# Optimization experiments

Hardware: AMD Instinct MI355X
Metric: run time of the kernel (lower is better)

The kernel has to match this reference:

```python
import jax, jax.numpy as jnp
import numpy as np

N_NODES = 50000
N_EDGES = 800000
IN_DIM = 128
HEADS = 8
HEAD_DIM = 16


def setup_inputs() -> dict:
    key = jax.random.key(0)
    ks = jax.random.split(key, 9)
    s = 1.0 / np.sqrt(IN_DIM)
    return {
        "h": jax.random.normal(ks[0], (N_NODES, IN_DIM), dtype=jnp.float32),
        "src": jax.random.randint(ks[1], (N_EDGES,), 0, N_NODES, dtype=jnp.int32),
        "dst": jax.random.randint(ks[2], (N_EDGES,), 0, N_NODES, dtype=jnp.int32),
        "WQ": jax.random.normal(ks[3], (IN_DIM, HEADS * HEAD_DIM), dtype=jnp.float32) * s,
        "bQ": jnp.zeros((HEADS * HEAD_DIM,), dtype=jnp.float32),
        "WK": jax.random.normal(ks[4], (IN_DIM, HEADS * HEAD_DIM), dtype=jnp.float32) * s,
        "bK": jnp.zeros((HEADS * HEAD_DIM,), dtype=jnp.float32),
        "WV": jax.random.normal(ks[5], (IN_DIM, HEADS * HEAD_DIM), dtype=jnp.float32) * s,
        "bV": jnp.zeros((HEADS * HEAD_DIM,), dtype=jnp.float32),
    }


def reference(h, src, dst, WQ, bQ, WK, bK, WV, bV):
    N = h.shape[0]
    sqrt_d = jnp.float32(np.sqrt(HEAD_DIM))
    # node projections, viewed as [N, H, D]
    Q = (h @ WQ + bQ).reshape(N, HEADS, HEAD_DIM)
    K = (h @ WK + bK).reshape(N, HEADS, HEAD_DIM)
    V = (h @ WV + bV).reshape(N, HEADS, HEAD_DIM)
    # edge scores: (K_src . Q_dst) per head, scaled exp with clamp [-5, 5]
    score = jnp.sum(K[src] * Q[dst], axis=-1, keepdims=True)  # [E, H, 1]
    score = jnp.exp(jnp.clip(score / sqrt_d, -5.0, 5.0))
    # segment-softmax denominator z and weighted V sum wV, both scattered to dst
    z = jax.ops.segment_sum(score, dst, num_segments=N)            # [N, H, 1]
    wV = jax.ops.segment_sum(V[src] * score, dst, num_segments=N)  # [N, H, D]
    # possible_empty: divide only where z > 0 (wV is 0 there anyway)
    head_out = jnp.where(z > 0, wV / jnp.where(z > 0, z, 1.0), wV)
    return head_out
```

## Files before the change

kernel.cpp:

```cpp
#include <hip/hip_runtime.h>
#include <math.h>

#define DIM 128
#define N_HEADS 8
#define HD 16
#define CAP 64

typedef __attribute__((ext_vector_type(8))) short bf16x8;
typedef __attribute__((ext_vector_type(4))) float f32x4;

__device__ __forceinline__ unsigned bf16pack2(float a, float b) {
    unsigned ua = __builtin_bit_cast(unsigned, a);
    unsigned ub = __builtin_bit_cast(unsigned, b);
    ua = (ua + 0x7FFFu + ((ua >> 16) & 1u)) >> 16;
    ub = (ub + 0x7FFFu + ((ub >> 16) & 1u)) >> 16;
    return ua | (ub << 16);
}
__device__ __forceinline__ float bf16lo(unsigned p) {
    return __builtin_bit_cast(float, p << 16);
}
__device__ __forceinline__ float bf16hi(unsigned p) {
    return __builtin_bit_cast(float, p & 0xFFFF0000u);
}

__global__ __launch_bounds__(256)
void init_kernel(const float* __restrict__ WQ, const float* __restrict__ bQ,
                 const float* __restrict__ WK, const float* __restrict__ bK,
                 const float* __restrict__ WV, const float* __restrict__ bV,
                 unsigned short* __restrict__ WT, float* __restrict__ bias384,
                 int* __restrict__ cnt, int NB, int N)
{
    if ((int)blockIdx.x < NB) {
        int i = blockIdx.x * 256 + threadIdx.x;
        if (i < N) cnt[i] = 0;
    } else {
        int idx = ((int)blockIdx.x - NB) * 256 + threadIdx.x;
        int c = idx >> 7, k = idx & 127;
        const float* W; const float* b; int col = c & 127;
        if (c < 128)      { W = WQ; b = bQ; }
        else if (c < 256) { W = WK; b = bK; }
        else              { W = WV; b = bV; }
        float v = W[k * DIM + col];
        WT[(size_t)c * DIM + k] = (unsigned short)(bf16pack2(v, 0.0f) & 0xFFFFu);
        if (k == 0) bias384[c] = b[col];
    }
}

__global__ __launch_bounds__(256)
void append_qkv_kernel(const int* __restrict__ src, const int* __restrict__ dst,
                       int* __restrict__ cnt, unsigned short* __restrict__ srcsF,
                       int E, int EB,
                       const float* __restrict__ h,
                       const unsigned short* __restrict__ WT,
                       const float* __restrict__ bias384,
                       unsigned* __restrict__ Qd, unsigned* __restrict__ KVd,
                       int N)
{
    __shared__ unsigned short hs[64 * 136];

    if ((int)blockIdx.x < EB) {
        int t = (blockIdx.x * 256 + threadIdx.x) * 4;
        if (t + 3 < E) {
            int4 d4 = *(const int4*)(dst + t);
            int4 s4 = *(const int4*)(src + t);
            int sl0 = atomicAdd(&cnt[d4.x], 1);
            int sl1 = atomicAdd(&cnt[d4.y], 1);
            int sl2 = atomicAdd(&cnt[d4.z], 1);
            int sl3 = atomicAdd(&cnt[d4.w], 1);
            if (sl0 < CAP) srcsF[(size_t)d4.x * CAP + sl0] = (unsigned short)s4.x;
            if (sl1 < CAP) srcsF[(size_t)d4.y * CAP + sl1] = (unsigned short)s4.y;
            if (sl2 < CAP) srcsF[(size_t)d4.z * CAP + sl2] = (unsigned short)s4.z;
            if (sl3 < CAP) srcsF[(size_t)d4.w * CAP + sl3] = (unsigned short)s4.w;
        } else {
            for (int e = t; e < E; ++e) {
                int d    = dst[e];
                int slot = atomicAdd(&cnt[d], 1);
                if (slot < CAP) srcsF[(size_t)d * CAP + slot] = (unsigned short)src[e];
            }
        }
        return;
    }

    const int tid = threadIdx.x;
    const int n0  = ((int)blockIdx.x - EB) * 64;

    #pragma unroll
    for (int i = 0; i < 4; ++i) {
        int lin  = i * 256 + tid;
        int node = lin >> 4;
        int k0   = (lin & 15) * 8;
        int gn   = n0 + node;
        float4 a0, a1;
        if (gn < N) {
            a0 = *(const float4*)(h + (size_t)gn * DIM + k0);
            a1 = *(const float4*)(h + (size_t)gn * DIM + k0 + 4);
        } else {
            a0 = make_float4(0.f, 0.f, 0.f, 0.f);
            a1 = a0;
        }
        uint4 p = make_uint4(bf16pack2(a0.x, a0.y), bf16pack2(a0.z, a0.w),
                             bf16pack2(a1.x, a1.y), bf16pack2(a1.z, a1.w));
        *(uint4*)(hs + node * 136 + k0) = p;
    }
    __syncthreads();

    const int wave   = tid >> 6;
    const int l      = tid & 63;
    const int lane16 = l & 15;
    const int quad   = l >> 4;
    const int wc0    = wave * 96;

    f32x4 acc[6][4];
    #pragma unroll
    for (int ct = 0; ct < 6; ++ct) {
        float4 bv = *(const float4*)(bias384 + wc0 + ct * 16 + quad * 4);
        #pragma unroll
        for (int rt = 0; rt < 4; ++rt)
            acc[ct][rt] = (f32x4){bv.x, bv.y, bv.z, bv.w};
    }

    #pragma unroll
    for (int ks = 0; ks < 4; ++ks) {
        bf16x8 a[6], b[4];
        #pragma unroll
        for (int ct = 0; ct < 6; ++ct)
            a[ct] = *(const bf16x8*)(WT + (size_t)(wc0 + ct * 16 + lane16) * DIM
                                         + ks * 32 + quad * 8);
        #pragma unroll
        for (int rt = 0; rt < 4; ++rt)
            b[rt] = *(const bf16x8*)(hs + (rt * 16 + lane16) * 136 + ks * 32 + quad * 8);
        #pragma unroll
        for (int ct = 0; ct < 6; ++ct)
            #pragma unroll
            for (int rt = 0; rt < 4; ++rt)
                acc[ct][rt] = __builtin_amdgcn_mfma_f32_16x16x32_bf16(
                    a[ct], b[rt], acc[ct][rt], 0, 0, 0);
    }

    #pragma unroll
    for (int ct = 0; ct < 6; ++ct) {
        const int col = wc0 + ct * 16 + quad * 4;
        #pragma unroll
        for (int rt = 0; rt < 4; ++rt) {
            int gn = n0 + rt * 16 + lane16;
            if (gn >= N) continue;
            f32x4 v = acc[ct][rt];
            uint2 pr = make_uint2(bf16pack2(v[0], v[1]), bf16pack2(v[2], v[3]));
            if (col < 128) {
                *(uint2*)(Qd + (size_t)gn * 64 + (col >> 1)) = pr;
            } else if (col < 256) {
                int c = col - 128;
                *(uint2*)(KVd + (size_t)gn * 128 + ((c >> 3) * 8) + ((c & 4) >> 1)) = pr;
            } else {
                int c = col - 256;
                *(uint2*)(KVd + (size_t)gn * 128 + ((c >> 3) * 8) + 4 + ((c & 4) >> 1)) = pr;
            }
        }
    }
}

__device__ __forceinline__ void issue_chunk(
    const unsigned* __restrict__ KVd, int bkt, int degc, int eg, int slot, int c,
    uint4 (&K)[4], uint4 (&V)[4])
{
    #pragma unroll
    for (int j = 0; j < 4; ++j) {
        int ee = eg + j * 4 + slot;
        int s  = __shfl(bkt, ee);
        s      = (ee < degc) ? s : 0;
        const uint4* p = (const uint4*)(KVd + (size_t)s * 128 + c * 8);
        K[j] = p[0];
        V[j] = p[1];
    }
}

__device__ __forceinline__ void compute_chunk(
    const uint4 (&K)[4], const uint4 (&V)[4], int eg, int degc, int slot,
    float q0, float q1, float q2, float q3,
    float q4, float q5, float q6, float q7,
    float acc[8], float& zs)
{
    float d[4];
    #pragma unroll
    for (int j = 0; j < 4; ++j)
        d[j] = bf16lo(K[j].x) * q0 + bf16hi(K[j].x) * q1
             + bf16lo(K[j].y) * q2 + bf16hi(K[j].y) * q3
             + bf16lo(K[j].z) * q4 + bf16hi(K[j].z) * q5
             + bf16lo(K[j].w) * q6 + bf16hi(K[j].w) * q7;
    #pragma unroll
    for (int j = 0; j < 4; ++j) d[j] += __shfl_xor(d[j], 1);

    #pragma unroll
    for (int j = 0; j < 4; ++j) {
        float pc = fminf(fmaxf(d[j] * 0.25f, -5.0f), 5.0f);
        float w  = ((eg + j * 4 + slot) < degc) ? __expf(pc) : 0.0f;
        zs += w;
        acc[0] += w * bf16lo(V[j].x); acc[1] += w * bf16hi(V[j].x);
        acc[2] += w * bf16lo(V[j].y); acc[3] += w * bf16hi(V[j].y);
        acc[4] += w * bf16lo(V[j].z); acc[5] += w * bf16hi(V[j].z);
        acc[6] += w * bf16lo(V[j].w); acc[7] += w * bf16hi(V[j].w);
    }
}

__global__ __launch_bounds__(256, 4)
void aggregate_kernel(const int* __restrict__ cnt,
                      const unsigned short* __restrict__ srcsF,
                      const unsigned* __restrict__ Qd,
                      const unsigned* __restrict__ KVd,
                      float* __restrict__ out, int N)
{
    const int l      = threadIdx.x & 63;
    const int slot   = l >> 4;
    const int c      = l & 15;
    const int stride = gridDim.x * 4;

    int node = blockIdx.x * 4 + (threadIdx.x >> 6);
    if (node >= N) return;

    int   deg = cnt[node];
    uint4 qd  = *(const uint4*)(Qd + (size_t)node * 64 + c * 4);
    int   bkt = srcsF[(size_t)node * CAP + l];

    uint4 K0[4], V0[4];
    issue_chunk(KVd, bkt, deg > CAP ? CAP : deg, 0, slot, c, K0, V0);

    for (;;) {
        const int  nn      = node + stride;
        const bool hasNext = nn < N;

        int ndeg = 0; uint4 nqd = make_uint4(0u, 0u, 0u, 0u); int nbkt = 0;
        if (hasNext) {
            ndeg = cnt[nn];
            nqd  = *(const uint4*)(Qd + (size_t)nn * 64 + c * 4);
            nbkt = srcsF[(size_t)nn * CAP + l];
        }

        const int degc = deg > CAP ? CAP : deg;

        uint4 K1[4], V1[4];
        const bool has1 = degc > 16;
        if (has1) issue_chunk(KVd, bkt, degc, 16, slot, c, K1, V1);

        const float q0 = bf16lo(qd.x), q1 = bf16hi(qd.x);
        const float q2 = bf16lo(qd.y), q3 = bf16hi(qd.y);
        const float q4 = bf16lo(qd.z), q5 = bf16hi(qd.z);
        const float q6 = bf16lo(qd.w), q7 = bf16hi(qd.w);

        float acc[8] = {0.f, 0.f, 0.f, 0.f, 0.f, 0.f, 0.f, 0.f};
        float zs = 0.f;

        compute_chunk(K0, V0, 0, degc, slot, q0, q1, q2, q3, q4, q5, q6, q7, acc, zs);
        if (has1)
            compute_chunk(K1, V1, 16, degc, slot, q0, q1, q2, q3, q4, q5, q6, q7, acc, zs);
        if (degc > 32) {
            issue_chunk(KVd, bkt, degc, 32, slot, c, K1, V1);
            compute_chunk(K1, V1, 32, degc, slot, q0, q1, q2, q3, q4, q5, q6, q7, acc, zs);
        }
        if (degc > 48) {
            issue_chunk(KVd, bkt, degc, 48, slot, c, K1, V1);
            compute_chunk(K1, V1, 48, degc, slot, q0, q1, q2, q3, q4, q5, q6, q7, acc, zs);
        }

        #pragma unroll
        for (int j = 0; j < 8; ++j) {
            acc[j] += __shfl_xor(acc[j], 16);
            acc[j] += __shfl_xor(acc[j], 32);
        }
        zs += __shfl_xor(zs, 16);
        zs += __shfl_xor(zs, 32);

        if (slot == 0) {
            float inv = (zs > 0.0f) ? (1.0f / zs) : 0.0f;
            f32x4 o0 = {acc[0] * inv, acc[1] * inv, acc[2] * inv, acc[3] * inv};
            f32x4 o1 = {acc[4] * inv, acc[5] * inv, acc[6] * inv, acc[7] * inv};
            __builtin_nontemporal_store(o0, (f32x4*)(out + (size_t)node * DIM + c * 8));
            __builtin_nontemporal_store(o1, (f32x4*)(out + (size_t)node * DIM + c * 8 + 4));
        }

        if (!hasNext) break;

        node = nn; deg = ndeg; qd = nqd; bkt = nbkt;
        issue_chunk(KVd, bkt, deg > CAP ? CAP : deg, 0, slot, c, K0, V0);
    }
}

extern "C" void kernel_launch(void* const* d_in, const int* in_sizes, int n_in,
                              void* d_out, int out_size, void* d_ws, size_t ws_size,
                              hipStream_t stream) {
    const float* h   = (const float*)d_in[0];
    const int*   src = (const int*)  d_in[1];
    const int*   dst = (const int*)  d_in[2];
    const float* WQ  = (const float*)d_in[3];
    const float* bQ  = (const float*)d_in[4];
    const float* WK  = (const float*)d_in[5];
    const float* bK  = (const float*)d_in[6];
    const float* WV  = (const float*)d_in[7];
    const float* bV  = (const float*)d_in[8];
    float* out = (float*)d_out;

    const int N  = in_sizes[0] / DIM;
    const int E  = in_sizes[1];
    const int NB = (N + 255) / 256;
    const int EB = (E / 4 + 255) / 256;
    const int QB = (N + 63) / 64;
    const int nConv = (384 * DIM) / 256;

    char* w = (char*)d_ws;
    unsigned*       Qd      = (unsigned*)w;        w += (size_t)N * 64  * sizeof(unsigned);
    unsigned*       KVd     = (unsigned*)w;        w += (size_t)N * 128 * sizeof(unsigned);
    unsigned short* WT      = (unsigned short*)w;  w += (size_t)384 * DIM * sizeof(unsigned short);
    float*          bias384 = (float*)w;           w += 384 * sizeof(float);
    int*            cnt     = (int*)w;             w += (size_t)N * sizeof(int);
    unsigned short* srcsF   = (unsigned short*)w;

    init_kernel<<<NB + nConv, 256, 0, stream>>>(WQ, bQ, WK, bK, WV, bV,
                                                WT, bias384, cnt, NB, N);
    append_qkv_kernel<<<EB + QB, 256, 0, stream>>>(src, dst, cnt, srcsF, E, EB,
                                                   h, WT, bias384, Qd, KVd, N);
    aggregate_kernel<<<2048, 256, 0, stream>>>(cnt, srcsF, Qd, KVd, out, N);
}
```

Before: 229.1 us.

## Store Q/K/V head-major and aggregate one head per block

The QKV projection now writes Q and interleaved K/V in head-major layout ([head][node][16]) instead of node-major. The aggregation kernel assigns each block to a single head (blockIdx & 7) and gives each wave a contiguous run of destination nodes, with 8 lanes per destination each handling one edge. The aim is to keep each head's K/V slab (about N*64 bytes) cache-resident, so random gathers hit L2/MALL more often. In exchange, per-lane register use rises (16 accumulators plus 16 q values), the launch-bounds occupancy hint is dropped, the srcsF index list is re-read once per head, and each lane now issues a separate gather per edge.

```diff
diff --git a/kernel.cpp b/kernel.cpp
--- a/kernel.cpp
+++ b/kernel.cpp
@@ -53,7 +53,7 @@
                        const float* __restrict__ h,
                        const unsigned short* __restrict__ WT,
                        const float* __restrict__ bias384,
-                       unsigned* __restrict__ Qd, unsigned* __restrict__ KVd,
+                       unsigned* __restrict__ Qh, unsigned* __restrict__ KVh,
                        int N)
 {
     __shared__ unsigned short hs[64 * 136];
@@ -147,140 +147,111 @@
             f32x4 v = acc[ct][rt];
             uint2 pr = make_uint2(bf16pack2(v[0], v[1]), bf16pack2(v[2], v[3]));
             if (col < 128) {
-                *(uint2*)(Qd + (size_t)gn * 64 + (col >> 1)) = pr;
+                int hq = col >> 4, d = col & 15;
+                *(uint2*)(Qh + ((size_t)hq * N + gn) * 8 + (d >> 1)) = pr;
             } else if (col < 256) {
-                int c = col - 128;
-                *(uint2*)(KVd + (size_t)gn * 128 + ((c >> 3) * 8) + ((c & 4) >> 1)) = pr;
+                int c = col - 128, hq = c >> 4, d = c & 15;
+                *(uint2*)(KVh + ((size_t)hq * N + gn) * 16 + (d >> 1)) = pr;
             } else {
-                int c = col - 256;
-                *(uint2*)(KVd + (size_t)gn * 128 + ((c >> 3) * 8) + 4 + ((c & 4) >> 1)) = pr;
+                int c = col - 256, hq = c >> 4, d = c & 15;
+                *(uint2*)(KVh + ((size_t)hq * N + gn) * 16 + 8 + (d >> 1)) = pr;
             }
         }
     }
 }
 
-__device__ __forceinline__ void issue_chunk(
-    const unsigned* __restrict__ KVd, int bkt, int degc, int eg, int slot, int c,
-    uint4 (&K)[4], uint4 (&V)[4])
-{
-    #pragma unroll
-    for (int j = 0; j < 4; ++j) {
-        int ee = eg + j * 4 + slot;
-        int s  = __shfl(bkt, ee);
-        s      = (ee < degc) ? s : 0;
-        const uint4* p = (const uint4*)(KVd + (size_t)s * 128 + c * 8);
-        K[j] = p[0];
-        V[j] = p[1];
-    }
-}
-
-__device__ __forceinline__ void compute_chunk(
-    const uint4 (&K)[4], const uint4 (&V)[4], int eg, int degc, int slot,
-    float q0, float q1, float q2, float q3,
-    float q4, float q5, float q6, float q7,
-    float acc[8], float& zs)
-{
-    float d[4];
-    #pragma unroll
-    for (int j = 0; j < 4; ++j)
-        d[j] = bf16lo(K[j].x) * q0 + bf16hi(K[j].x) * q1
-             + bf16lo(K[j].y) * q2 + bf16hi(K[j].y) * q3
-             + bf16lo(K[j].z) * q4 + bf16hi(K[j].z) * q5
-             + bf16lo(K[j].w) * q6 + bf16hi(K[j].w) * q7;
-    #pragma unroll
-    for (int j = 0; j < 4; ++j) d[j] += __shfl_xor(d[j], 1);
-
-    #pragma unroll
-    for (int j = 0; j < 4; ++j) {
-        float pc = fminf(fmaxf(d[j] * 0.25f, -5.0f), 5.0f);
-        float w  = ((eg + j * 4 + slot) < degc) ? __expf(pc) : 0.0f;
-        zs += w;
-        acc[0] += w * bf16lo(V[j].x); acc[1] += w * bf16hi(V[j].x);
-        acc[2] += w * bf16lo(V[j].y); acc[3] += w * bf16hi(V[j].y);
-        acc[4] += w * bf16lo(V[j].z); acc[5] += w * bf16hi(V[j].z);
-        acc[6] += w * bf16lo(V[j].w); acc[7] += w * bf16hi(V[j].w);
-    }
-}
-
-__global__ __launch_bounds__(256, 4)
+__global__ __launch_bounds__(256)
 void aggregate_kernel(const int* __restrict__ cnt,
                       const unsigned short* __restrict__ srcsF,
-                      const unsigned* __restrict__ Qd,
-                      const unsigned* __restrict__ KVd,
+                      const unsigned* __restrict__ Qh,
+                      const unsigned* __restrict__ KVh,
                       float* __restrict__ out, int N)
 {
-    const int l      = threadIdx.x & 63;
-    const int slot   = l >> 4;
-    const int c      = l & 15;
-    const int stride = gridDim.x * 4;
-
-    int node = blockIdx.x * 4 + (threadIdx.x >> 6);
-    if (node >= N) return;
-
-    int   deg = cnt[node];
-    uint4 qd  = *(const uint4*)(Qd + (size_t)node * 64 + c * 4);
-    int   bkt = srcsF[(size_t)node * CAP + l];
-
-    uint4 K0[4], V0[4];
-    issue_chunk(KVd, bkt, deg > CAP ? CAP : deg, 0, slot, c, K0, V0);
-
-    for (;;) {
-        const int  nn      = node + stride;
-        const bool hasNext = nn < N;
-
-        int ndeg = 0; uint4 nqd = make_uint4(0u, 0u, 0u, 0u); int nbkt = 0;
-        if (hasNext) {
-            ndeg = cnt[nn];
-            nqd  = *(const uint4*)(Qd + (size_t)nn * 64 + c * 4);
-            nbkt = srcsF[(size_t)nn * CAP + l];
-        }
-
-        const int degc = deg > CAP ? CAP : deg;
-
-        uint4 K1[4], V1[4];
-        const bool has1 = degc > 16;
-        if (has1) issue_chunk(KVd, bkt, degc, 16, slot, c, K1, V1);
-
-        const float q0 = bf16lo(qd.x), q1 = bf16hi(qd.x);
-        const float q2 = bf16lo(qd.y), q3 = bf16hi(qd.y);
-        const float q4 = bf16lo(qd.z), q5 = bf16hi(qd.z);
-        const float q6 = bf16lo(qd.w), q7 = bf16hi(qd.w);
-
-        float acc[8] = {0.f, 0.f, 0.f, 0.f, 0.f, 0.f, 0.f, 0.f};
-        float zs = 0.f;
-
-        compute_chunk(K0, V0, 0, degc, slot, q0, q1, q2, q3, q4, q5, q6, q7, acc, zs);
-        if (has1)
-            compute_chunk(K1, V1, 16, degc, slot, q0, q1, q2, q3, q4, q5, q6, q7, acc, zs);
-        if (degc > 32) {
-            issue_chunk(KVd, bkt, degc, 32, slot, c, K1, V1);
-            compute_chunk(K1, V1, 32, degc, slot, q0, q1, q2, q3, q4, q5, q6, q7, acc, zs);
-        }
-        if (degc > 48) {
-            issue_chunk(KVd, bkt, degc, 48, slot, c, K1, V1);
-            compute_chunk(K1, V1, 48, degc, slot, q0, q1, q2, q3, q4, q5, q6, q7, acc, zs);
-        }
-
-        #pragma unroll
-        for (int j = 0; j < 8; ++j) {
-            acc[j] += __shfl_xor(acc[j], 16);
-            acc[j] += __shfl_xor(acc[j], 32);
-        }
-        zs += __shfl_xor(zs, 16);
-        zs += __shfl_xor(zs, 32);
-
-        if (slot == 0) {
-            float inv = (zs > 0.0f) ? (1.0f / zs) : 0.0f;
-            f32x4 o0 = {acc[0] * inv, acc[1] * inv, acc[2] * inv, acc[3] * inv};
-            f32x4 o1 = {acc[4] * inv, acc[5] * inv, acc[6] * inv, acc[7] * inv};
-            __builtin_nontemporal_store(o0, (f32x4*)(out + (size_t)node * DIM + c * 8));
-            __builtin_nontemporal_store(o1, (f32x4*)(out + (size_t)node * DIM + c * 8 + 4));
-        }
-
-        if (!hasNext) break;
-
-        node = nn; deg = ndeg; qd = nqd; bkt = nbkt;
-        issue_chunk(KVd, bkt, deg > CAP ? CAP : deg, 0, slot, c, K0, V0);
+    const int hh   = blockIdx.x & 7;
+    const int wseq = ((int)blockIdx.x >> 3) * 4 + (threadIdx.x >> 6);
+    const int lane = threadIdx.x & 63;
+    const int dloc = lane >> 3;
+    const int slot = lane & 7;
+
+    const int RUN   = (N + 1023) >> 10;
+    const int start = wseq * RUN;
+    const int end   = (start + RUN < N) ? (start + RUN) : N;
+    const size_t hN = (size_t)hh * N;
+
+    for (int d0 = start; d0 < end; d0 += 8) {
+        const int  myDst = d0 + dloc;
+        const bool vd    = myDst < end;
+        const int  aDst  = vd ? myDst : start;
+        int deg = vd ? cnt[aDst] : 0;
+        if (deg > CAP) deg = CAP;
+
+        const uint4* qp = (const uint4*)(Qh + (hN + aDst) * 8);
+        uint4 qa = qp[0], qb = qp[1];
+        float q[16];
+        q[0]  = bf16lo(qa.x); q[1]  = bf16hi(qa.x);
+        q[2]  = bf16lo(qa.y); q[3]  = bf16hi(qa.y);
+        q[4]  = bf16lo(qa.z); q[5]  = bf16hi(qa.z);
+        q[6]  = bf16lo(qa.w); q[7]  = bf16hi(qa.w);
+        q[8]  = bf16lo(qb.x); q[9]  = bf16hi(qb.x);
+        q[10] = bf16lo(qb.y); q[11] = bf16hi(qb.y);
+        q[12] = bf16lo(qb.z); q[13] = bf16hi(qb.z);
+        q[14] = bf16lo(qb.w); q[15] = bf16hi(qb.w);
+
+        float acc[16];
+        #pragma unroll
+        for (int k = 0; k < 16; ++k) acc[k] = 0.f;
+        float z = 0.f;
+
+        for (int base = 0; base < CAP; base += 8) {
+            int  e   = base + slot;
+            bool val = e < deg;
+            if (!__any(val)) break;
+            int s = val ? (int)srcsF[(size_t)aDst * CAP + e] : 0;
+
+            const uint4* kv = (const uint4*)(KVh + (hN + s) * 16);
+            uint4 K0 = kv[0], K1 = kv[1], V0 = kv[2], V1 = kv[3];
+
+            float d = bf16lo(K0.x) * q[0]  + bf16hi(K0.x) * q[1]
+                    + bf16lo(K0.y) * q[2]  + bf16hi(K0.y) * q[3]
+                    + bf16lo(K0.z) * q[4]  + bf16hi(K0.z) * q[5]
+                    + bf16lo(K0.w) * q[6]  + bf16hi(K0.w) * q[7]
+                    + bf16lo(K1.x) * q[8]  + bf16hi(K1.x) * q[9]
+                    + bf16lo(K1.y) * q[10] + bf16hi(K1.y) * q[11]
+                    + bf16lo(K1.z) * q[12] + bf16hi(K1.z) * q[13]
+                    + bf16lo(K1.w) * q[14] + bf16hi(K1.w) * q[15];
+
+            float pc = fminf(fmaxf(d * 0.25f, -5.0f), 5.0f);
+            float w  = val ? __expf(pc) : 0.0f;
+            z += w;
+            acc[0]  += w * bf16lo(V0.x); acc[1]  += w * bf16hi(V0.x);
+            acc[2]  += w * bf16lo(V0.y); acc[3]  += w * bf16hi(V0.y);
+            acc[4]  += w * bf16lo(V0.z); acc[5]  += w * bf16hi(V0.z);
+            acc[6]  += w * bf16lo(V0.w); acc[7]  += w * bf16hi(V0.w);
+            acc[8]  += w * bf16lo(V1.x); acc[9]  += w * bf16hi(V1.x);
+            acc[10] += w * bf16lo(V1.y); acc[11] += w * bf16hi(V1.y);
+            acc[12] += w * bf16lo(V1.z); acc[13] += w * bf16hi(V1.z);
+            acc[14] += w * bf16lo(V1.w); acc[15] += w * bf16hi(V1.w);
+        }
+
+        #pragma unroll
+        for (int m = 1; m <= 4; m <<= 1) {
+            z += __shfl_xor(z, m);
+            #pragma unroll
+            for (int k = 0; k < 16; ++k) acc[k] += __shfl_xor(acc[k], m);
+        }
+
+        if (slot == 0 && vd) {
+            float inv = (z > 0.0f) ? (1.0f / z) : 0.0f;
+            float* op = out + (size_t)myDst * DIM + hh * HD;
+            f32x4 o0 = {acc[0] * inv,  acc[1] * inv,  acc[2] * inv,  acc[3] * inv};
+            f32x4 o1 = {acc[4] * inv,  acc[5] * inv,  acc[6] * inv,  acc[7] * inv};
+            f32x4 o2 = {acc[8] * inv,  acc[9] * inv,  acc[10] * inv, acc[11] * inv};
+            f32x4 o3 = {acc[12] * inv, acc[13] * inv, acc[14] * inv, acc[15] * inv};
+            __builtin_nontemporal_store(o0, (f32x4*)(op));
+            __builtin_nontemporal_store(o1, (f32x4*)(op + 4));
+            __builtin_nontemporal_store(o2, (f32x4*)(op + 8));
+            __builtin_nontemporal_store(o3, (f32x4*)(op + 12));
+        }
     }
 }
 
@@ -306,8 +277,8 @@
     const int nConv = (384 * DIM) / 256;
 
     char* w = (char*)d_ws;
-    unsigned*       Qd      = (unsigned*)w;        w += (size_t)N * 64  * sizeof(unsigned);
-    unsigned*       KVd     = (unsigned*)w;        w += (size_t)N * 128 * sizeof(unsigned);
+    unsigned*       Qh      = (unsigned*)w;        w += (size_t)N * 64  * sizeof(unsigned);
+    unsigned*       KVh     = (unsigned*)w;        w += (size_t)N * 128 * sizeof(unsigned);
     unsigned short* WT      = (unsigned short*)w;  w += (size_t)384 * DIM * sizeof(unsigned short);
     float*          bias384 = (float*)w;           w += 384 * sizeof(float);
     int*            cnt     = (int*)w;             w += (size_t)N * sizeof(int);
@@ -316,6 +287,6 @@
     init_kernel<<<NB + nConv, 256, 0, stream>>>(WQ, bQ, WK, bK, WV, bV,
                                                 WT, bias384, cnt, NB, N);
     append_qkv_kernel<<<EB + QB, 256, 0, stream>>>(src, dst, cnt, srcsF, E, EB,
-                                                   h, WT, bias384, Qd, KVd, N);
-    aggregate_kernel<<<2048, 256, 0, stream>>>(cnt, srcsF, Qd, KVd, out, N);
-}
+                                                   h, WT, bias384, Qh, KVh, N);
+    aggregate_kernel<<<2048, 256, 0, stream>>>(cnt, srcsF, Qh, KVh, out, N);
+}
```

Measured after the change: 242.1 us. 1.06x slower.
